# Kernel tuning notes

Measured on AMD Instinct MI355X. Metric: run time of the kernel, lower is better.

The kernel has to match this reference:

```python
import jax, jax.numpy as jnp
import numpy as np


def setup_inputs() -> dict:
    key = jax.random.key(0)
    ks = jax.random.split(key, 5)
    B, T, D, E = 4, 2048, 1024, 8
    inputs = jax.random.normal(ks[0], (B, T, D), dtype=jnp.float32)
    Wr = jax.random.normal(ks[1], (D, E), dtype=jnp.float32) * 0.02
    br = jnp.zeros((E,), dtype=jnp.float32)
    W1 = jax.random.normal(ks[2], (E, D, D), dtype=jnp.float32) * 0.02
    b1 = jnp.zeros((E, D), dtype=jnp.float32)
    W2 = jax.random.normal(ks[3], (E, D, D), dtype=jnp.float32) * 0.02
    b2 = jnp.zeros((E, D), dtype=jnp.float32)
    return {"inputs": inputs, "Wr": Wr, "br": br, "W1": W1, "b1": b1, "W2": W2, "b2": b2}


def reference(inputs, Wr, br, W1, b1, W2, b2):
    B, T, D = inputs.shape
    E = Wr.shape[1]
    x = inputs.reshape(B * T, D)            # [N, D]
    N = x.shape[0]
    C = N // E                              # expert capacity

    # --- Router (top-1), inference path (no training noise) ---
    logits = x @ Wr + br                    # [N, E]
    probs = jax.nn.softmax(logits, axis=-1)
    gate = jnp.max(probs, axis=-1, keepdims=True)     # [N, 1] expert_gate
    idx = jnp.argmax(probs, axis=-1)                  # [N]
    mask = jax.nn.one_hot(idx, E, dtype=jnp.float32)  # [N, E]

    # 1-based position of each token within its chosen expert (0 elsewhere)
    pos = (jnp.cumsum(mask, axis=0) * mask).astype(jnp.int32)  # [N, E]
    # capacity check uses the 1-based position (faithful to original)
    mask = mask * (pos < C).astype(jnp.float32)
    mask_flat = jnp.sum(mask, axis=-1, keepdims=True)          # [N, 1]
    gate = gate * mask_flat                                    # [N, 1]

    # combine tensor [N, E, C]; slots for non-chosen experts (pos==0 -> one_hot slot 0)
    # are zeroed by the gate*one_hot(idx) factor, as in the original.
    combine = (gate * mask_flat * jax.nn.one_hot(idx, E, dtype=jnp.float32))[..., None] \
              * jax.nn.one_hot(pos, C, dtype=jnp.float32)      # [N, E, C]
    dispatch = combine                                         # float32 cast is identity

    # --- Dispatch: dense einsum (faithful to original anti-pattern) ---
    expert_in = jnp.einsum('nd,nec->ecd', x, dispatch)         # [E, C, D]

    # --- Per-expert FFN as grouped GEMM: Dense(D, relu) -> Dense(D) ---
    h = jax.nn.relu(jnp.einsum('ecd,edf->ecf', expert_in, W1) + b1[:, None, :])
    eo = jnp.einsum('ecf,efd->ecd', h, W2) + b2[:, None, :]    # [E, C, D]

    # --- Combine ---
    out = jnp.einsum('ecd,nec->nd', eo, combine)               # [N, D]
    return out.reshape(B, T, D)
```

## Files before the change

### kernel.cpp

```cpp
#include <hip/hip_runtime.h>
#include <hip/hip_bf16.h>
#include <stdint.h>

#define N_TOK 8192
#define DIM   1024
#define NEXP  8
#define CAP   1024

typedef __attribute__((ext_vector_type(8))) short bf16x8;
typedef __attribute__((ext_vector_type(4))) float f32x4;

static __device__ __forceinline__ unsigned short f2bf(float f) {
  unsigned int u = __float_as_uint(f);
  u += 0x7FFFu + ((u >> 16) & 1u);
  return (unsigned short)(u >> 16);
}

static __device__ __forceinline__ void gld_lds16(const void* g, void* l) {
  __builtin_amdgcn_global_load_lds(
      (__attribute__((address_space(1))) void*)(uintptr_t)g,
      (__attribute__((address_space(3))) void*)(unsigned int)(uintptr_t)l,
      16, 0, 0);
}

__global__ void router_kernel(const float* __restrict__ x, const float* __restrict__ Wr,
                              const float* __restrict__ br, float* __restrict__ gate,
                              int* __restrict__ idxs) {
  const int wid  = (blockIdx.x * blockDim.x + threadIdx.x) >> 6;
  const int lane = threadIdx.x & 63;
  const float* xr = x + (size_t)wid * DIM;
  double acc[8] = {0,0,0,0,0,0,0,0};
  #pragma unroll 4
  for (int j = 0; j < 16; ++j) {
    const int d = j * 64 + lane;
    const double xv = (double)xr[d];
    const float4 wa = *(const float4*)(Wr + d * 8);
    const float4 wb = *(const float4*)(Wr + d * 8 + 4);
    acc[0] += xv * (double)wa.x;  acc[1] += xv * (double)wa.y;
    acc[2] += xv * (double)wa.z;  acc[3] += xv * (double)wa.w;
    acc[4] += xv * (double)wb.x;  acc[5] += xv * (double)wb.y;
    acc[6] += xv * (double)wb.z;  acc[7] += xv * (double)wb.w;
  }
  #pragma unroll
  for (int off = 1; off < 64; off <<= 1) {
    #pragma unroll
    for (int e = 0; e < 8; ++e) acc[e] += __shfl_xor(acc[e], off);
  }
  if (lane == 0) {
    double lg[8];
    #pragma unroll
    for (int e = 0; e < 8; ++e) lg[e] = acc[e] + (double)br[e];
    int best = 0; double bm = lg[0];
    #pragma unroll
    for (int e = 1; e < 8; ++e) { if (lg[e] > bm) { bm = lg[e]; best = e; } }
    double s = 0.0;
    #pragma unroll
    for (int e = 0; e < 8; ++e) s += exp(lg[e] - bm);
    gate[wid] = (float)(1.0 / s);
    idxs[wid] = best;
  }
}

__global__ void scan_kernel(const int* __restrict__ idxs, int* __restrict__ slot_token,
                            int* __restrict__ keep) {
  __shared__ int wtot[16][8];
  const int t = threadIdx.x, lane = t & 63, w = t >> 6;
  #pragma unroll
  for (int j = 0; j < 8; ++j) slot_token[t * 8 + j] = -1;
  int myidx[8];
  #pragma unroll
  for (int j = 0; j < 8; ++j) myidx[j] = idxs[t * 8 + j];
  int cnt[8], incl[8];
  #pragma unroll
  for (int e = 0; e < 8; ++e) {
    int c = 0;
    #pragma unroll
    for (int j = 0; j < 8; ++j) c += (myidx[j] == e) ? 1 : 0;
    cnt[e] = c;
    int v = c;
    #pragma unroll
    for (int off = 1; off < 64; off <<= 1) {
      int u = __shfl_up(v, off);
      if (lane >= off) v += u;
    }
    incl[e] = v;
  }
  if (lane == 63) {
    #pragma unroll
    for (int e = 0; e < 8; ++e) wtot[w][e] = incl[e];
  }
  __syncthreads();
  if (t == 0) {
    int run[8] = {0,0,0,0,0,0,0,0};
    for (int ww = 0; ww < 16; ++ww) {
      #pragma unroll
      for (int e = 0; e < 8; ++e) {
        int tmp = wtot[ww][e]; wtot[ww][e] = run[e]; run[e] += tmp;
      }
    }
  }
  __syncthreads();
  #pragma unroll
  for (int e = 0; e < 8; ++e) {
    int r = wtot[w][e] + incl[e] - cnt[e];
    #pragma unroll
    for (int j = 0; j < 8; ++j) {
      if (myidx[j] == e) {
        ++r;
        const int kept = (r < CAP) ? 1 : 0;
        keep[t * 8 + j] = kept;
        if (kept) slot_token[e * CAP + r] = t * 8 + j;
      }
    }
  }
}

__global__ void gather_zero_kernel(const float* __restrict__ x, const float* __restrict__ gate,
                                   const int* __restrict__ slot_token,
                                   const int* __restrict__ keep,
                                   unsigned short* __restrict__ Xe,
                                   float* __restrict__ out) {
  const int t = threadIdx.x;
  if (blockIdx.x < NEXP * CAP) {
    const int s = blockIdx.x;
    const int n = slot_token[s];
    if (n < 0) return;
    const float g = gate[n];
    const float4 v = ((const float4*)(x + (size_t)n * DIM))[t];
    ushort4 o;
    o.x = f2bf(v.x * g); o.y = f2bf(v.y * g); o.z = f2bf(v.z * g); o.w = f2bf(v.w * g);
    ((ushort4*)(Xe + (size_t)s * DIM))[t] = o;
  } else {
    const int n = blockIdx.x - NEXP * CAP;
    if (keep[n]) return;
    float4 z = {0.f, 0.f, 0.f, 0.f};
    ((float4*)(out + (size_t)n * DIM))[t] = z;
  }
}

__global__ void wt_kernel(const float* __restrict__ W1, const float* __restrict__ W2,
                          unsigned short* __restrict__ W1T, unsigned short* __restrict__ W2T) {
  __shared__ float tile[32][33];
  const int mi = blockIdx.y;
  const int tz = blockIdx.x;
  const int tr = tz >> 5, tc = tz & 31;
  const float* src = (mi < 8) ? (W1 + (size_t)mi * DIM * DIM)
                              : (W2 + (size_t)(mi - 8) * DIM * DIM);
  unsigned short* dst = (mi < 8) ? (W1T + (size_t)mi * DIM * DIM)
                                 : (W2T + (size_t)(mi - 8) * DIM * DIM);
  const int t = threadIdx.x;
  const int row = t >> 3;
  const int cg  = (t & 7) * 4;
  const float4 v = *(const float4*)(src + (size_t)(tr * 32 + row) * DIM + tc * 32 + cg);
  tile[row][cg + 0] = v.x; tile[row][cg + 1] = v.y;
  tile[row][cg + 2] = v.z; tile[row][cg + 3] = v.w;
  __syncthreads();
  ushort4 o;
  o.x = f2bf(tile[cg + 0][row]); o.y = f2bf(tile[cg + 1][row]);
  o.z = f2bf(tile[cg + 2][row]); o.w = f2bf(tile[cg + 3][row]);
  *(ushort4*)(dst + (size_t)(tc * 32 + row) * DIM + tr * 32 + cg) = o;
}

template <int OP>
__global__ __launch_bounds__(256)
void gemm_kernel(const unsigned short* __restrict__ A,
                 const unsigned short* __restrict__ Bt,
                 const float* __restrict__ bias,
                 const int* __restrict__ slot_token,
                 const float* __restrict__ gate,
                 unsigned short* __restrict__ Hout,
                 float* __restrict__ Cout)
{
  __shared__ unsigned short Asub[2][128 * 32];
  __shared__ unsigned short Bsub[2][128 * 32];
  const int bid = blockIdx.x;
  const int e  = bid & 7;
  const int tt = bid >> 3;
  const int bm = tt >> 3;
  const int bn = tt & 7;
  const int tid = threadIdx.x, lane = tid & 63, w = tid >> 6;
  const int wr = w >> 1, wc = w & 1;

  const unsigned short* Ae = A  + (size_t)(e * CAP + bm * 128) * DIM;
  const unsigned short* Be = Bt + (size_t)e * DIM * DIM + (size_t)(bn * 128) * DIM;

  const int srow = lane >> 2;
  const int scol = (lane & 3) * 8;
  const int lrow = lane & 15;
  const int kof  = (lane >> 4) * 8;

  f32x4 acc[4][4] = {};

  auto stage = [&](int buf, int kt) {
    const int k0 = kt * 32;
    #pragma unroll
    for (int c = 0; c < 2; ++c) {
      const int chunk = w + c * 4;
      const int r = chunk * 16 + srow;
      gld_lds16(Ae + (size_t)r * DIM + k0 + scol, &Asub[buf][chunk * 512]);
      gld_lds16(Be + (size_t)r * DIM + k0 + scol, &Bsub[buf][chunk * 512]);
    }
  };
  auto compute = [&](int buf) {
    bf16x8 af[4], bfr[4];
    #pragma unroll
    for (int m = 0; m < 4; ++m)
      af[m] = *(const bf16x8*)&Asub[buf][(wr * 64 + m * 16 + lrow) * 32 + kof];
    #pragma unroll
    for (int n = 0; n < 4; ++n)
      bfr[n] = *(const bf16x8*)&Bsub[buf][(wc * 64 + n * 16 + lrow) * 32 + kof];
    #pragma unroll
    for (int m = 0; m < 4; ++m)
      #pragma unroll
      for (int n = 0; n < 4; ++n)
        acc[m][n] = __builtin_amdgcn_mfma_f32_16x16x32_bf16(af[m], bfr[n], acc[m][n], 0, 0, 0);
  };

  stage(0, 0);
  __syncthreads();
  int cur = 0;
  for (int kt = 0; kt < 31; ++kt) {
    stage(cur ^ 1, kt + 1);
    compute(cur);
    __syncthreads();
    cur ^= 1;
  }
  compute(cur);

  if (OP == 1) {
    #pragma unroll
    for (int n = 0; n < 4; ++n) {
      const int col = bn * 128 + wc * 64 + n * 16 + lrow;
      const float bv = bias[e * DIM + col];
      #pragma unroll
      for (int m = 0; m < 4; ++m) {
        const int r0 = bm * 128 + wr * 64 + m * 16 + (lane >> 4) * 4;
        #pragma unroll
        for (int i = 0; i < 4; ++i) {
          float v = acc[m][n][i] + bv;
          v = v > 0.0f ? v : 0.0f;
          Hout[(size_t)(e * CAP + r0 + i) * DIM + col] = f2bf(v);
        }
      }
    }
  } else {
    float bv[4];
    #pragma unroll
    for (int n = 0; n < 4; ++n)
      bv[n] = bias[e * DIM + bn * 128 + wc * 64 + n * 16 + lrow];
    #pragma unroll
    for (int m = 0; m < 4; ++m) {
      const int r0 = bm * 128 + wr * 64 + m * 16 + (lane >> 4) * 4;
      #pragma unroll
      for (int i = 0; i < 4; ++i) {
        const int tok = slot_token[e * CAP + r0 + i];
        if (tok >= 0) {
          const float g = gate[tok];
          float* orow = Cout + (size_t)tok * DIM;
          #pragma unroll
          for (int n = 0; n < 4; ++n) {
            const int col = bn * 128 + wc * 64 + n * 16 + lrow;
            orow[col] = g * (acc[m][n][i] + bv[n]);
          }
        }
      }
    }
  }
}

extern "C" void kernel_launch(void* const* d_in, const int* in_sizes, int n_in,
                              void* d_out, int out_size, void* d_ws, size_t ws_size,
                              hipStream_t stream) {
  const float* x  = (const float*)d_in[0];
  const float* Wr = (const float*)d_in[1];
  const float* br = (const float*)d_in[2];
  const float* W1 = (const float*)d_in[3];
  const float* b1 = (const float*)d_in[4];
  const float* W2 = (const float*)d_in[5];
  const float* b2 = (const float*)d_in[6];
  float* out = (float*)d_out;

  char* ws = (char*)d_ws;
  unsigned short* Xe  = (unsigned short*)(ws);
  unsigned short* Hh  = (unsigned short*)(ws + (size_t)16 * 1024 * 1024);
  unsigned short* W1T = (unsigned short*)(ws + (size_t)32 * 1024 * 1024);
  unsigned short* W2T = (unsigned short*)(ws + (size_t)48 * 1024 * 1024);
  float* gate     = (float*)(ws + (size_t)64 * 1024 * 1024);
  int*   idxs     = (int*)  (ws + (size_t)64 * 1024 * 1024 + 32768);
  int*   slot_tok = (int*)  (ws + (size_t)64 * 1024 * 1024 + 65536);
  int*   keep     = (int*)  (ws + (size_t)64 * 1024 * 1024 + 98304);

  router_kernel<<<2048, 256, 0, stream>>>(x, Wr, br, gate, idxs);
  scan_kernel<<<1, 1024, 0, stream>>>(idxs, slot_tok, keep);
  gather_zero_kernel<<<2 * N_TOK, 256, 0, stream>>>(x, gate, slot_tok, keep, Xe, out);
  wt_kernel<<<dim3(1024, 16), 256, 0, stream>>>(W1, W2, W1T, W2T);
  gemm_kernel<1><<<512, 256, 0, stream>>>(Xe, W1T, b1, nullptr, nullptr, Hh, nullptr);
  gemm_kernel<2><<<512, 256, 0, stream>>>(Hh, W2T, b2, slot_tok, gate, nullptr, out);
}
```

Before: 241.4 us.

## Triple-buffer GEMM K-loop and merge weight-transpose with gather kernel

Moves the GEMM main loop from double to triple buffering in LDS. Tiles are prefetched two iterations ahead, and explicit vmcnt waits plus raw s_barrier replace __syncthreads, so global loads overlap compute with fewer full drains. The weight transpose/convert kernel and the gather/zero kernel are also merged into one launch to cut a kernel boundary. The cost is 50% more LDS per block, which may lower occupancy, and the vmcnt counts rely on each stage issuing exactly 4 loads per thread.

```diff
diff --git a/kernel.cpp b/kernel.cpp
--- a/kernel.cpp
+++ b/kernel.cpp
@@ -115,14 +115,33 @@
   }
 }
 
-__global__ void gather_zero_kernel(const float* __restrict__ x, const float* __restrict__ gate,
-                                   const int* __restrict__ slot_token,
-                                   const int* __restrict__ keep,
-                                   unsigned short* __restrict__ Xe,
-                                   float* __restrict__ out) {
+__global__ void util_kernel(const float* __restrict__ W1, const float* __restrict__ W2,
+                            unsigned short* __restrict__ W1T, unsigned short* __restrict__ W2T,
+                            const float* __restrict__ x, const float* __restrict__ gate,
+                            const int* __restrict__ slot_token, const int* __restrict__ keep,
+                            unsigned short* __restrict__ Xe, float* __restrict__ out) {
   const int t = threadIdx.x;
-  if (blockIdx.x < NEXP * CAP) {
-    const int s = blockIdx.x;
+  if (blockIdx.x < 16384) {
+    __shared__ float tile[32][33];
+    const int mi = blockIdx.x >> 10;
+    const int tz = blockIdx.x & 1023;
+    const int tr = tz >> 5, tc = tz & 31;
+    const float* src = (mi < 8) ? (W1 + (size_t)mi * DIM * DIM)
+                                : (W2 + (size_t)(mi - 8) * DIM * DIM);
+    unsigned short* dst = (mi < 8) ? (W1T + (size_t)mi * DIM * DIM)
+                                   : (W2T + (size_t)(mi - 8) * DIM * DIM);
+    const int row = t >> 3;
+    const int cg  = (t & 7) * 4;
+    const float4 v = *(const float4*)(src + (size_t)(tr * 32 + row) * DIM + tc * 32 + cg);
+    tile[row][cg + 0] = v.x; tile[row][cg + 1] = v.y;
+    tile[row][cg + 2] = v.z; tile[row][cg + 3] = v.w;
+    __syncthreads();
+    ushort4 o;
+    o.x = f2bf(tile[cg + 0][row]); o.y = f2bf(tile[cg + 1][row]);
+    o.z = f2bf(tile[cg + 2][row]); o.w = f2bf(tile[cg + 3][row]);
+    *(ushort4*)(dst + (size_t)(tc * 32 + row) * DIM + tr * 32 + cg) = o;
+  } else if (blockIdx.x < 16384 + NEXP * CAP) {
+    const int s = blockIdx.x - 16384;
     const int n = slot_token[s];
     if (n < 0) return;
     const float g = gate[n];
@@ -131,34 +150,11 @@
     o.x = f2bf(v.x * g); o.y = f2bf(v.y * g); o.z = f2bf(v.z * g); o.w = f2bf(v.w * g);
     ((ushort4*)(Xe + (size_t)s * DIM))[t] = o;
   } else {
-    const int n = blockIdx.x - NEXP * CAP;
+    const int n = blockIdx.x - (16384 + NEXP * CAP);
     if (keep[n]) return;
     float4 z = {0.f, 0.f, 0.f, 0.f};
     ((float4*)(out + (size_t)n * DIM))[t] = z;
   }
-}
-
-__global__ void wt_kernel(const float* __restrict__ W1, const float* __restrict__ W2,
-                          unsigned short* __restrict__ W1T, unsigned short* __restrict__ W2T) {
-  __shared__ float tile[32][33];
-  const int mi = blockIdx.y;
-  const int tz = blockIdx.x;
-  const int tr = tz >> 5, tc = tz & 31;
-  const float* src = (mi < 8) ? (W1 + (size_t)mi * DIM * DIM)
-                              : (W2 + (size_t)(mi - 8) * DIM * DIM);
-  unsigned short* dst = (mi < 8) ? (W1T + (size_t)mi * DIM * DIM)
-                                 : (W2T + (size_t)(mi - 8) * DIM * DIM);
-  const int t = threadIdx.x;
-  const int row = t >> 3;
-  const int cg  = (t & 7) * 4;
-  const float4 v = *(const float4*)(src + (size_t)(tr * 32 + row) * DIM + tc * 32 + cg);
-  tile[row][cg + 0] = v.x; tile[row][cg + 1] = v.y;
-  tile[row][cg + 2] = v.z; tile[row][cg + 3] = v.w;
-  __syncthreads();
-  ushort4 o;
-  o.x = f2bf(tile[cg + 0][row]); o.y = f2bf(tile[cg + 1][row]);
-  o.z = f2bf(tile[cg + 2][row]); o.w = f2bf(tile[cg + 3][row]);
-  *(ushort4*)(dst + (size_t)(tc * 32 + row) * DIM + tr * 32 + cg) = o;
 }
 
 template <int OP>
@@ -171,8 +167,8 @@
                  unsigned short* __restrict__ Hout,
                  float* __restrict__ Cout)
 {
-  __shared__ unsigned short Asub[2][128 * 32];
-  __shared__ unsigned short Bsub[2][128 * 32];
+  __shared__ unsigned short Asub[3][128 * 32];
+  __shared__ unsigned short Bsub[3][128 * 32];
   const int bid = blockIdx.x;
   const int e  = bid & 7;
   const int tt = bid >> 3;
@@ -217,15 +213,19 @@
   };
 
   stage(0, 0);
-  __syncthreads();
-  int cur = 0;
-  for (int kt = 0; kt < 31; ++kt) {
-    stage(cur ^ 1, kt + 1);
-    compute(cur);
-    __syncthreads();
-    cur ^= 1;
-  }
-  compute(cur);
+  stage(1, 1);
+  asm volatile("s_waitcnt vmcnt(4)" ::: "memory");
+  __builtin_amdgcn_s_barrier();
+  int b0 = 0, b1 = 1, b2 = 2;
+  for (int kt = 0; kt < 32; ++kt) {
+    if (kt < 30) stage(b2, kt + 2);
+    compute(b0);
+    if (kt == 31) break;
+    if (kt < 30) asm volatile("s_waitcnt vmcnt(4)" ::: "memory");
+    else         asm volatile("s_waitcnt vmcnt(0)" ::: "memory");
+    __builtin_amdgcn_s_barrier();
+    const int tb = b0; b0 = b1; b1 = b2; b2 = tb;
+  }
 
   if (OP == 1) {
     #pragma unroll
@@ -292,8 +292,7 @@
 
   router_kernel<<<2048, 256, 0, stream>>>(x, Wr, br, gate, idxs);
   scan_kernel<<<1, 1024, 0, stream>>>(idxs, slot_tok, keep);
-  gather_zero_kernel<<<2 * N_TOK, 256, 0, stream>>>(x, gate, slot_tok, keep, Xe, out);
-  wt_kernel<<<dim3(1024, 16), 256, 0, stream>>>(W1, W2, W1T, W2T);
+  util_kernel<<<32768, 256, 0, stream>>>(W1, W2, W1T, W2T, x, gate, slot_tok, keep, Xe, out);
   gemm_kernel<1><<<512, 256, 0, stream>>>(Xe, W1T, b1, nullptr, nullptr, Hh, nullptr);
   gemm_kernel<2><<<512, 256, 0, stream>>>(Hh, W2T, b2, slot_tok, gate, nullptr, out);
 }
```

Result: faster. 234.9 us (-2.7%).
